# Optimization experiments

Hardware: AMD Instinct MI355X
Metric: run time of the kernel (lower is better)

Reference implementation:

```python
import jax, jax.numpy as jnp
import numpy as np

N, E, IN, H, G = 100000, 1600000, 64, 108, 128
N_LAYERS = 2  # hidden_dims=[108,108] -> 1 layer from hidden_dims[1:] + 1 final layer


def setup_inputs() -> dict:
    key = jax.random.key(0)
    ks = jax.random.split(key, 13)
    s = lambda fan_in: 1.0 / np.sqrt(fan_in)
    inp = {
        "nodes_feat": jax.random.normal(ks[0], (N, IN), jnp.float32),
        "edges_feat": jax.random.normal(ks[1], (E, 1), jnp.float32),
        "nodes_num_norm_sqrt": jax.random.uniform(ks[2], (N,), jnp.float32),
        "edges_num_norm_sqrt": jax.random.uniform(ks[3], (E,), jnp.float32),
        "W_emb": jax.random.uniform(ks[4], (IN, H), jnp.float32, -s(IN), s(IN)),
        "b_emb": jax.random.uniform(ks[5], (H,), jnp.float32, -s(IN), s(IN)),
        "pool_W": jax.random.uniform(ks[6], (N_LAYERS, H, H), jnp.float32, -s(H), s(H)),
        "pool_b": jax.random.uniform(ks[7], (N_LAYERS, H), jnp.float32, -s(H), s(H)),
        "app_W": jax.random.uniform(ks[8], (N_LAYERS, 2 * H, H), jnp.float32, -s(2 * H), s(2 * H)),
        "app_b": jax.random.uniform(ks[9], (N_LAYERS, H), jnp.float32, -s(2 * H), s(2 * H)),
        "src": jax.random.randint(ks[10], (E,), 0, N, jnp.int64 if jax.config.jax_enable_x64 else jnp.int32),
        "dst": jax.random.randint(ks[11], (E,), 0, N, jnp.int64 if jax.config.jax_enable_x64 else jnp.int32),
        "graph_ids": jnp.sort(jax.random.randint(ks[12], (N,), 0, G, jnp.int64 if jax.config.jax_enable_x64 else jnp.int32)),
        "n_graphs": G,
    }
    return inp


def reference(nodes_feat, edges_feat, nodes_num_norm_sqrt, edges_num_norm_sqrt,
              W_emb, b_emb, pool_W, pool_b, app_W, app_b,
              src, dst, graph_ids, n_graphs):
    n = nodes_feat.shape[0]
    # embedding_h
    h = nodes_feat @ W_emb + b_emb  # [N, H]
    # in-degree for mean aggregation (dropout = 0.0 so omitted)
    deg = jax.ops.segment_sum(jnp.ones((src.shape[0],), h.dtype), dst, num_segments=n)
    deg = jnp.maximum(deg, 1.0)[:, None]  # [N, 1]
    for i in range(pool_W.shape[0]):
        h_in = h
        # meanpool aggregator: per-message linear+ReLU == per-node transform then gather
        z = jax.nn.relu(h @ pool_W[i] + pool_b[i])  # [N, H]
        c = jax.ops.segment_sum(z[src], dst, num_segments=n) / deg  # mean over neighbors
        # NodeApply: linear(concat(h, c)) -> L2 normalize -> activation
        b = jnp.concatenate([h, c], axis=1) @ app_W[i] + app_b[i]
        b = b / jnp.maximum(jnp.linalg.norm(b, axis=1, keepdims=True), 1e-12)
        h = h_in + jax.nn.relu(b)  # residual (dims match: 108 == 108)
    # dgl.mean_nodes readout per graph
    cnt = jax.ops.segment_sum(jnp.ones((n,), h.dtype), graph_ids, num_segments=n_graphs)
    hg = jax.ops.segment_sum(h, graph_ids, num_segments=n_graphs) / jnp.maximum(cnt, 1.0)[:, None]
    return hg  # [n_graphs, H]
```

## Files before the change

kernel.cpp:

```cpp
#include <hip/hip_runtime.h>

#define HDIM 108
constexpr int G_GRAPHS = 128;
constexpr int MAXNB = 1024;
constexpr int CAP = 2560;

typedef _Float16 half8 __attribute__((ext_vector_type(8)));
typedef _Float16 half4v __attribute__((ext_vector_type(4)));
typedef float floatx4 __attribute__((ext_vector_type(4)));
typedef float floatx2 __attribute__((ext_vector_type(2)));

__device__ inline unsigned char f32_to_fp8(float t) {
#if __has_builtin(__builtin_amdgcn_cvt_pk_fp8_f32)
  return (unsigned char)(__builtin_amdgcn_cvt_pk_fp8_f32(t, t, 0, false) & 0xFF);
#else
  t = fminf(t, 448.f);
  if (t < 0.015625f) return (unsigned char)__float2int_rn(t * 512.f);
  unsigned u = __float_as_uint(t);
  unsigned lsb = (u >> 20) & 1;
  u += 0x7FFFFu + lsb;
  int e = (int)((u >> 23) & 0xFF) - 127;
  if (e > 8) return 0x7E;
  return (unsigned char)(((e + 7) << 3) | ((u >> 20) & 7));
#endif
}

template <bool HI>
__device__ inline floatx2 fp8x2_to_f32(unsigned v) {
#if __has_builtin(__builtin_amdgcn_cvt_pk_f32_fp8)
  return __builtin_amdgcn_cvt_pk_f32_fp8((int)v, HI);
#else
  unsigned b0 = HI ? ((v >> 16) & 0xFF) : (v & 0xFF);
  unsigned b1 = HI ? ((v >> 24) & 0xFF) : ((v >> 8) & 0xFF);
  floatx2 r;
  {
    unsigned s = b0 >> 7, e = (b0 >> 3) & 0xF, m = b0 & 7;
    float f = (e == 0) ? (float)m * 0.001953125f
                       : __uint_as_float(((e + 120u) << 23) | (m << 20));
    r[0] = s ? -f : f;
  }
  {
    unsigned s = b1 >> 7, e = (b1 >> 3) & 0xF, m = b1 & 7;
    float f = (e == 0) ? (float)m * 0.001953125f
                       : __uint_as_float(((e + 120u) << 23) | (m << 20));
    r[1] = s ? -f : f;
  }
  return r;
#endif
}

__global__ __launch_bounds__(1024) void k_fused0(const int* __restrict__ src, const int* __restrict__ dst,
                                                 int* __restrict__ gcur, int* __restrict__ ebuf,
                                                 const float* __restrict__ pool_W,
                                                 const float* __restrict__ app_W,
                                                 _Float16* __restrict__ wtp,
                                                 _Float16* __restrict__ wta,
                                                 const float* __restrict__ feat,
                                                 const float* __restrict__ W_emb,
                                                 const float* __restrict__ b_emb,
                                                 _Float16* __restrict__ h16,
                                                 int E, int nb, int nsc, int N) {
  __shared__ __align__(16) char smraw[29440];
  const int tid = threadIdx.x;

  if ((int)blockIdx.x < nsc) {
    int* hist = (int*)smraw;
    const int e0 = blockIdx.x * 16384;

    int gi = blockIdx.x * 1024 + tid;
    if (gi < 78848) {
      const float* srcw;
      _Float16* dstw;
      int Kpad, split, rel;
      if (gi < 14336)      { rel = gi;          srcw = pool_W;         dstw = wtp;         Kpad = 128; split = 0; }
      else if (gi < 28672) { rel = gi - 14336;  srcw = pool_W + 11664; dstw = wtp + 14336; Kpad = 128; split = 0; }
      else if (gi < 53760) { rel = gi - 28672;  srcw = app_W;          dstw = wta;         Kpad = 224; split = 1; }
      else                 { rel = gi - 53760;  srcw = app_W + 23328;  dstw = wta + 25088; Kpad = 224; split = 1; }
      int n = rel / Kpad, k = rel - n * Kpad;
      int ks;
      if (split) ks = (k < 108) ? k : (k >= 112 && k < 220) ? (k - 4) : -1;
      else       ks = (k < 108) ? k : -1;
      float v = (n < 108 && ks >= 0) ? srcw[ks * 108 + n] : 0.f;
      dstw[rel] = (_Float16)v;
    }

    for (int b = tid; b < nb; b += 1024) hist[b] = 0;
    __syncthreads();
#pragma unroll
    for (int it = 0; it < 16; it++) {
      int e = e0 + it * 1024 + tid;
      if (e < E) atomicAdd(&hist[dst[e] >> 7], 1);
    }
    __syncthreads();
    for (int b = tid; b < nb; b += 1024) {
      int h = hist[b];
      hist[b] = h ? atomicAdd(&gcur[b * 16], h) : 0;
    }
    __syncthreads();
#pragma unroll
    for (int it = 0; it < 16; it++) {
      int e = e0 + it * 1024 + tid;
      if (e < E) {
        int d = dst[e];
        int b = d >> 7;
        int rank = atomicAdd(&hist[b], 1);
        if (rank < CAP) ebuf[(size_t)b * CAP + rank] = src[e] | ((d & 127) << 20);
      }
    }
  } else {
    _Float16* As = (_Float16*)smraw;
    _Float16* Ws = (_Float16*)(smraw + 20480);
    const int sub = tid >> 8;
    const int stid = tid & 255;
    const int swave = stid >> 6;
    const int slane = stid & 63;
    const int lo = slane & 15;
    const int quad = slane >> 4;
    const int n0 = (((int)blockIdx.x - nsc) * 4 + sub) * 64;

    floatx4 acc[7];
#pragma unroll
    for (int ct = 0; ct < 7; ct++) {
      floatx4 zz = {0.f, 0.f, 0.f, 0.f};
      acc[ct] = zz;
    }

#pragma unroll 1
    for (int kc = 0; kc < 2; kc++) {
      {
        int r = stid >> 2, sg = stid & 3;
        int gn = n0 + r;
        int k = kc * 32 + sg * 8;
        half8 v = {0, 0, 0, 0, 0, 0, 0, 0};
        if (gn < N) {
          float4 f0 = *(const float4*)(feat + (size_t)gn * 64 + k);
          float4 f1 = *(const float4*)(feat + (size_t)gn * 64 + k + 4);
          v[0] = (_Float16)f0.x; v[1] = (_Float16)f0.y; v[2] = (_Float16)f0.z; v[3] = (_Float16)f0.w;
          v[4] = (_Float16)f1.x; v[5] = (_Float16)f1.y; v[6] = (_Float16)f1.z; v[7] = (_Float16)f1.w;
        }
        *(half8*)&As[sub * 2560 + r * 40 + sg * 8] = v;
      }
      if (tid < 448) {
        int nrow = tid >> 2, sg = tid & 3;
        int kb = kc * 32 + sg * 8;
        half8 v = {0, 0, 0, 0, 0, 0, 0, 0};
        if (nrow < 108) {
#pragma unroll
          for (int j = 0; j < 8; j++) v[j] = (_Float16)W_emb[(kb + j) * 108 + nrow];
        }
        *(half8*)&Ws[nrow * 40 + sg * 8] = v;
      }
      __syncthreads();

      half8 a = *(const half8*)&As[sub * 2560 + (swave * 16 + lo) * 40 + quad * 8];
#pragma unroll
      for (int ct = 0; ct < 7; ct++) {
        half8 b = *(const half8*)&Ws[(ct * 16 + lo) * 40 + quad * 8];
        acc[ct] = __builtin_amdgcn_mfma_f32_16x16x32_f16(a, b, acc[ct], 0, 0, 0);
      }
      __syncthreads();
    }

    float bias_v[7];
#pragma unroll
    for (int ct = 0; ct < 7; ct++) {
      int col = ct * 16 + lo;
      bias_v[ct] = (col < 108) ? b_emb[col] : 0.f;
    }
#pragma unroll
    for (int reg = 0; reg < 4; reg++) {
      int gr = n0 + swave * 16 + quad * 4 + reg;
      if (gr < N) {
        _Float16* op = h16 + (size_t)gr * 112 + lo;
#pragma unroll
        for (int ct = 0; ct < 7; ct++) {
          float t = acc[ct][reg] + bias_v[ct];
          op[ct * 16] = (_Float16)t;
        }
      }
    }
  }
}

__global__ __launch_bounds__(1024) void k_bagg(const unsigned char* __restrict__ z, const int* __restrict__ ebuf,
                                               const int* __restrict__ gcur, _Float16* __restrict__ c16,
                                               int N, int nb) {
  __shared__ int cnts[128];
  __shared__ int scanb[128];
  __shared__ int off[129];
  __shared__ int ecur[128];
  __shared__ int esrc[CAP];
  const int tid = threadIdx.x;
  const int b = blockIdx.x;
  const int v0 = b << 7;
  int cntb = gcur[b * 16];
  if (cntb > CAP) cntb = CAP;
  const int* eb = ebuf + (size_t)b * CAP;

  if (tid < 128) cnts[tid] = 0;
  __syncthreads();
  for (int i = tid; i < cntb; i += 1024) atomicAdd(&cnts[eb[i] >> 20], 1);
  __syncthreads();
  if (tid < 128) scanb[tid] = cnts[tid];
  __syncthreads();
#pragma unroll
  for (int st = 1; st < 128; st <<= 1) {
    int v = 0;
    if (tid < 128 && tid >= st) v = scanb[tid - st];
    __syncthreads();
    if (tid < 128) scanb[tid] += v;
    __syncthreads();
  }
  if (tid == 0) off[0] = 0;
  if (tid < 128) {
    off[tid + 1] = scanb[tid];
    ecur[tid] = scanb[tid] - cnts[tid];
  }
  __syncthreads();
  for (int i = tid; i < cntb; i += 1024) {
    int e = eb[i];
    int p = atomicAdd(&ecur[e >> 20], 1);
    esrc[p] = e & 0xFFFFF;
  }
  __syncthreads();

  const int lane = tid & 31;
  const int grp = tid >> 5;
  if (lane >= 28) return;
  const unsigned char* __restrict__ zl = z + lane * 4;
#pragma unroll 1
  for (int r = grp; r < 128; r += 32) {
    int v = v0 + r;
    if (v >= N) continue;
    int s = off[r], e2 = off[r + 1];
    float a0 = 0.f, a1 = 0.f, a2 = 0.f, a3 = 0.f;
    int j = s;
    for (; j + 4 <= e2; j += 4) {
      unsigned q0 = *(const unsigned*)(zl + (size_t)esrc[j] * 128);
      unsigned q1 = *(const unsigned*)(zl + (size_t)esrc[j + 1] * 128);
      unsigned q2 = *(const unsigned*)(zl + (size_t)esrc[j + 2] * 128);
      unsigned q3 = *(const unsigned*)(zl + (size_t)esrc[j + 3] * 128);
      floatx2 l0 = fp8x2_to_f32<false>(q0), h0 = fp8x2_to_f32<true>(q0);
      floatx2 l1 = fp8x2_to_f32<false>(q1), h1 = fp8x2_to_f32<true>(q1);
      floatx2 l2 = fp8x2_to_f32<false>(q2), h2 = fp8x2_to_f32<true>(q2);
      floatx2 l3 = fp8x2_to_f32<false>(q3), h3 = fp8x2_to_f32<true>(q3);
      a0 += (l0[0] + l1[0]) + (l2[0] + l3[0]);
      a1 += (l0[1] + l1[1]) + (l2[1] + l3[1]);
      a2 += (h0[0] + h1[0]) + (h2[0] + h3[0]);
      a3 += (h0[1] + h1[1]) + (h2[1] + h3[1]);
    }
    for (; j < e2; j++) {
      unsigned q0 = *(const unsigned*)(zl + (size_t)esrc[j] * 128);
      floatx2 l0 = fp8x2_to_f32<false>(q0), h0 = fp8x2_to_f32<true>(q0);
      a0 += l0[0]; a1 += l0[1]; a2 += h0[0]; a3 += h0[1];
    }
    int d = e2 - s;
    float inv = 1.f / (float)(d > 0 ? d : 1);
    half4v r4;
    r4[0] = (_Float16)(a0 * inv); r4[1] = (_Float16)(a1 * inv);
    r4[2] = (_Float16)(a2 * inv); r4[3] = (_Float16)(a3 * inv);
    *(half4v*)(c16 + (size_t)v * 112 + lane * 4) = r4;
  }
}

template <int KCH, int MODE>
__global__ __launch_bounds__(256) void k_mmf(const void* Asrc, const _Float16* __restrict__ c16,
                                             const _Float16* __restrict__ Wt, const float* __restrict__ bias,
                                             void* outp, int N) {
  constexpr int KW = KCH * 32;
  __shared__ _Float16 As[64 * 40];
  __shared__ _Float16 Ws[112 * 40];

  const int tid = threadIdx.x;
  const int wave = tid >> 6;
  const int lane = tid & 63;
  const int lo = lane & 15;
  const int quad = lane >> 4;
  const int n0 = blockIdx.x * 64;
  const _Float16* h16 = (const _Float16*)Asrc;

  floatx4 acc[7];
#pragma unroll
  for (int ct = 0; ct < 7; ct++) {
    floatx4 zz = {0.f, 0.f, 0.f, 0.f};
    acc[ct] = zz;
  }

#pragma unroll 1
  for (int kc = 0; kc < KCH; kc++) {
    {
      int r = tid >> 2, sg = tid & 3;
      int gn = n0 + r;
      int k = kc * 32 + sg * 8;
      half8 v = {0, 0, 0, 0, 0, 0, 0, 0};
      if (gn < N) {
        if (MODE == 2) {
          const _Float16* sp = (k < 112) ? (h16 + (size_t)gn * 112 + k)
                                         : (c16 + (size_t)gn * 112 + (k - 112));
          v = *(const half8*)sp;
        } else {
          if (k < 112) v = *(const half8*)(h16 + (size_t)gn * 112 + k);
        }
      }
      *(half8*)&As[r * 40 + sg * 8] = v;
    }
#pragma unroll
    for (int it = 0; it < 2; it++) {
      int idx = tid + it * 256;
      if (idx < 448) {
        int nrow = idx >> 2, sg = idx & 3;
        half8 v = *(const half8*)(Wt + (size_t)nrow * KW + kc * 32 + sg * 8);
        *(half8*)&Ws[nrow * 40 + sg * 8] = v;
      }
    }
    __syncthreads();

    half8 a = *(const half8*)&As[(wave * 16 + lo) * 40 + quad * 8];
#pragma unroll
    for (int ct = 0; ct < 7; ct++) {
      half8 b = *(const half8*)&Ws[(ct * 16 + lo) * 40 + quad * 8];
      acc[ct] = __builtin_amdgcn_mfma_f32_16x16x32_f16(a, b, acc[ct], 0, 0, 0);
    }
    __syncthreads();
  }

  float bias_v[7];
#pragma unroll
  for (int ct = 0; ct < 7; ct++) {
    int col = ct * 16 + lo;
    bias_v[ct] = (col < 108) ? bias[col] : 0.f;
  }

  if (MODE == 2) {
    _Float16* out16 = (_Float16*)outp;
#pragma unroll
    for (int reg = 0; reg < 4; reg++) {
      int gr = n0 + wave * 16 + quad * 4 + reg;
      float bv[7];
      float ssq = 0.f;
#pragma unroll
      for (int ct = 0; ct < 7; ct++) {
        float t = acc[ct][reg] + bias_v[ct];
        bv[ct] = t;
        ssq += t * t;
      }
#pragma unroll
      for (int s = 1; s < 16; s <<= 1) ssq += __shfl_xor(ssq, s, 16);
      float scale = 1.f / fmaxf(sqrtf(ssq), 1e-12f);
      if (gr < N) {
        _Float16* hp = out16 + (size_t)gr * 112 + lo;
#pragma unroll
        for (int ct = 0; ct < 7; ct++) {
          float hv = (float)hp[ct * 16];
          hp[ct * 16] = (_Float16)(hv + fmaxf(bv[ct] * scale, 0.f));
        }
      }
    }
  } else {
    unsigned char* outb = (unsigned char*)outp;
#pragma unroll
    for (int reg = 0; reg < 4; reg++) {
      int gr = n0 + wave * 16 + quad * 4 + reg;
      if (gr < N) {
        unsigned char* op = outb + (size_t)gr * 128 + lo;
#pragma unroll
        for (int ct = 0; ct < 7; ct++) {
          float t = fmaxf(acc[ct][reg] + bias_v[ct], 0.f);
          op[ct * 16] = f32_to_fp8(t);
        }
      }
    }
  }
}

__global__ __launch_bounds__(256) void k_readout(const _Float16* __restrict__ h, const int* __restrict__ gid,
                                                 float* __restrict__ hg, int N) {
  const int CH = 16;
  const int lane = threadIdx.x & 31;
  const int grp = threadIdx.x >> 5;
  int start = (blockIdx.x * 8 + grp) * CH;
  if (start >= N || lane >= 27) return;
  int end = min(start + CH, N);
  float a0 = 0.f, a1 = 0.f, a2 = 0.f, a3 = 0.f;
  int cur = gid[start];
  for (int i = start; i < end; i++) {
    int g = gid[i];
    if (g != cur) {
      float* base = &hg[(size_t)cur * HDIM + lane * 4];
      atomicAdd(base + 0, a0); atomicAdd(base + 1, a1);
      atomicAdd(base + 2, a2); atomicAdd(base + 3, a3);
      a0 = a1 = a2 = a3 = 0.f;
      cur = g;
    }
    half4v v = *(const half4v*)(h + (size_t)i * 112 + lane * 4);
    a0 += (float)v[0]; a1 += (float)v[1]; a2 += (float)v[2]; a3 += (float)v[3];
  }
  float* base = &hg[(size_t)cur * HDIM + lane * 4];
  atomicAdd(base + 0, a0); atomicAdd(base + 1, a1);
  atomicAdd(base + 2, a2); atomicAdd(base + 3, a3);
}

__global__ __launch_bounds__(256) void k_div(const float* __restrict__ hg, const int* __restrict__ gid,
                                             float* __restrict__ out, int total, int N) {
  int i = blockIdx.x * 256 + threadIdx.x;
  if (i < total) {
    int g = i / HDIM;
    int lo = 0, hi = N;
    while (lo < hi) { int m = (lo + hi) >> 1; if (gid[m] < g) lo = m + 1; else hi = m; }
    int lb = lo;
    lo = 0; hi = N;
    while (lo < hi) { int m = (lo + hi) >> 1; if (gid[m] <= g) lo = m + 1; else hi = m; }
    int c = lo - lb;
    out[i] = hg[i] / (float)(c > 0 ? c : 1);
  }
}

extern "C" void kernel_launch(void* const* d_in, const int* in_sizes, int n_in,
                              void* d_out, int out_size, void* d_ws, size_t ws_size,
                              hipStream_t stream) {
  (void)n_in; (void)ws_size; (void)out_size;
  const float* nodes_feat = (const float*)d_in[0];
  const float* W_emb = (const float*)d_in[4];
  const float* b_emb = (const float*)d_in[5];
  const float* pool_W = (const float*)d_in[6];
  const float* pool_b = (const float*)d_in[7];
  const float* app_W = (const float*)d_in[8];
  const float* app_b = (const float*)d_in[9];
  const int* src = (const int*)d_in[10];
  const int* dst = (const int*)d_in[11];
  const int* gid = (const int*)d_in[12];
  const int N = in_sizes[2];
  const int E = in_sizes[10];
  float* out = (float*)d_out;

  const int nb = (N + 127) >> 7;
  const int nbMM = (N + 63) / 64;
  const int nsc = (E + 16383) / 16384;
  const int ngb = (nbMM + 3) / 4;

  char* ws = (char*)d_ws;
  size_t off = 0;
  auto alloc = [&](size_t bytes) -> size_t {
    size_t o = off;
    off += (bytes + 1023) & ~size_t(1023);
    return o;
  };
  size_t o_gcur = alloc((size_t)MAXNB * 16 * 4);
  size_t o_hg   = alloc((size_t)G_GRAPHS * HDIM * 4);
  size_t zero_bytes = off;
  size_t o_ebuf = alloc((size_t)MAXNB * CAP * 4);
  size_t o_h  = alloc((size_t)N * 112 * 2);
  size_t o_z  = alloc((size_t)N * 128);
  size_t o_c  = alloc((size_t)N * 112 * 2);
  size_t o_wp = alloc((size_t)2 * 112 * 128 * 2);
  size_t o_wa = alloc((size_t)2 * 112 * 224 * 2);

  int*           gcur = (int*)(ws + o_gcur);
  float*         hg   = (float*)(ws + o_hg);
  int*           ebuf = (int*)(ws + o_ebuf);
  _Float16*      h16  = (_Float16*)(ws + o_h);
  unsigned char* z8   = (unsigned char*)(ws + o_z);
  _Float16*      c16  = (_Float16*)(ws + o_c);
  _Float16*      wtp  = (_Float16*)(ws + o_wp);
  _Float16*      wta  = (_Float16*)(ws + o_wa);

  (void)hipMemsetAsync(d_ws, 0, zero_bytes, stream);

  k_fused0<<<nsc + ngb, 1024, 0, stream>>>(src, dst, gcur, ebuf,
                                           pool_W, app_W, wtp, wta,
                                           nodes_feat, W_emb, b_emb, h16,
                                           E, nb, nsc, N);

  for (int i = 0; i < 2; i++) {
    k_mmf<4, 1><<<nbMM, 256, 0, stream>>>(h16, nullptr, wtp + i * 14336,
                                          pool_b + i * HDIM, z8, N);
    k_bagg<<<nb, 1024, 0, stream>>>(z8, ebuf, gcur, c16, N, nb);
    k_mmf<7, 2><<<nbMM, 256, 0, stream>>>(h16, c16, wta + i * 25088,
                                          app_b + i * HDIM, h16, N);
  }

  k_readout<<<(N + 8 * 16 - 1) / (8 * 16), 256, 0, stream>>>(h16, gid, hg, N);
  k_div<<<(G_GRAPHS * HDIM + 255) / 256, 256, 0, stream>>>(hg, gid, out, G_GRAPHS * HDIM, N);
}
```

Measured before the change: 328.6 us.

## Double-buffer LDS tiles in k_mmf and halve k_bagg block size

The matmul kernel now uses two LDS buffers. The next K-chunk of A and W is loaded into registers while the MFMAs run on the current chunk, which removes one barrier per iteration and hides global-load latency. The aggregation kernel drops from 1024 to 512 threads per block, with each wave group handling twice as many rows, which may improve occupancy or scheduling. Double buffering doubles LDS use and raises register pressure, and the smaller bagg blocks have less parallelism per block.

New measurement: 312.1 us. -5.0%, faster.

```diff
diff --git a/kernel.cpp b/kernel.cpp
--- a/kernel.cpp
+++ b/kernel.cpp
@@ -182,9 +182,9 @@
   }
 }
 
-__global__ __launch_bounds__(1024) void k_bagg(const unsigned char* __restrict__ z, const int* __restrict__ ebuf,
-                                               const int* __restrict__ gcur, _Float16* __restrict__ c16,
-                                               int N, int nb) {
+__global__ __launch_bounds__(512) void k_bagg(const unsigned char* __restrict__ z, const int* __restrict__ ebuf,
+                                              const int* __restrict__ gcur, _Float16* __restrict__ c16,
+                                              int N, int nb) {
   __shared__ int cnts[128];
   __shared__ int scanb[128];
   __shared__ int off[129];
@@ -199,7 +199,7 @@
 
   if (tid < 128) cnts[tid] = 0;
   __syncthreads();
-  for (int i = tid; i < cntb; i += 1024) atomicAdd(&cnts[eb[i] >> 20], 1);
+  for (int i = tid; i < cntb; i += 512) atomicAdd(&cnts[eb[i] >> 20], 1);
   __syncthreads();
   if (tid < 128) scanb[tid] = cnts[tid];
   __syncthreads();
@@ -217,7 +217,7 @@
     ecur[tid] = scanb[tid] - cnts[tid];
   }
   __syncthreads();
-  for (int i = tid; i < cntb; i += 1024) {
+  for (int i = tid; i < cntb; i += 512) {
     int e = eb[i];
     int p = atomicAdd(&ecur[e >> 20], 1);
     esrc[p] = e & 0xFFFFF;
@@ -229,7 +229,7 @@
   if (lane >= 28) return;
   const unsigned char* __restrict__ zl = z + lane * 4;
 #pragma unroll 1
-  for (int r = grp; r < 128; r += 32) {
+  for (int r = grp; r < 128; r += 16) {
     int v = v0 + r;
     if (v >= N) continue;
     int s = off[r], e2 = off[r + 1];
@@ -268,8 +268,8 @@
                                              const _Float16* __restrict__ Wt, const float* __restrict__ bias,
                                              void* outp, int N) {
   constexpr int KW = KCH * 32;
-  __shared__ _Float16 As[64 * 40];
-  __shared__ _Float16 Ws[112 * 40];
+  __shared__ _Float16 As[2][64 * 40];
+  __shared__ _Float16 Ws[2][112 * 40];
 
   const int tid = threadIdx.x;
   const int wave = tid >> 6;
@@ -279,6 +279,37 @@
   const int n0 = blockIdx.x * 64;
   const _Float16* h16 = (const _Float16*)Asrc;
 
+  const int ar = tid >> 2, asg = tid & 3;
+  const int gnA = n0 + ar;
+  const int wrow0 = tid >> 2, wsg0 = tid & 3;
+  const int widx1 = tid + 256;
+  const int wrow1 = widx1 >> 2, wsg1 = widx1 & 3;
+
+  auto loadA = [&](int kc) -> half8 {
+    int k = kc * 32 + asg * 8;
+    half8 v = {0, 0, 0, 0, 0, 0, 0, 0};
+    if (gnA < N) {
+      if (MODE == 2) {
+        const _Float16* sp = (k < 112) ? (h16 + (size_t)gnA * 112 + k)
+                                       : (c16 + (size_t)gnA * 112 + (k - 112));
+        v = *(const half8*)sp;
+      } else {
+        if (k < 112) v = *(const half8*)(h16 + (size_t)gnA * 112 + k);
+      }
+    }
+    return v;
+  };
+
+  half8 aR = loadA(0);
+  half8 wR0 = *(const half8*)(Wt + (size_t)wrow0 * KW + wsg0 * 8);
+  half8 wR1 = {0, 0, 0, 0, 0, 0, 0, 0};
+  if (tid < 192) wR1 = *(const half8*)(Wt + (size_t)wrow1 * KW + wsg1 * 8);
+
+  *(half8*)&As[0][ar * 40 + asg * 8] = aR;
+  *(half8*)&Ws[0][wrow0 * 40 + wsg0 * 8] = wR0;
+  if (tid < 192) *(half8*)&Ws[0][wrow1 * 40 + wsg1 * 8] = wR1;
+  __syncthreads();
+
   floatx4 acc[7];
 #pragma unroll
   for (int ct = 0; ct < 7; ct++) {
@@ -288,40 +319,26 @@
 
 #pragma unroll 1
   for (int kc = 0; kc < KCH; kc++) {
-    {
-      int r = tid >> 2, sg = tid & 3;
-      int gn = n0 + r;
-      int k = kc * 32 + sg * 8;
-      half8 v = {0, 0, 0, 0, 0, 0, 0, 0};
-      if (gn < N) {
-        if (MODE == 2) {
-          const _Float16* sp = (k < 112) ? (h16 + (size_t)gn * 112 + k)
-                                         : (c16 + (size_t)gn * 112 + (k - 112));
-          v = *(const half8*)sp;
-        } else {
-          if (k < 112) v = *(const half8*)(h16 + (size_t)gn * 112 + k);
-        }
-      }
-      *(half8*)&As[r * 40 + sg * 8] = v;
-    }
-#pragma unroll
-    for (int it = 0; it < 2; it++) {
-      int idx = tid + it * 256;
-      if (idx < 448) {
-        int nrow = idx >> 2, sg = idx & 3;
-        half8 v = *(const half8*)(Wt + (size_t)nrow * KW + kc * 32 + sg * 8);
-        *(half8*)&Ws[nrow * 40 + sg * 8] = v;
-      }
-    }
-    __syncthreads();
-
-    half8 a = *(const half8*)&As[(wave * 16 + lo) * 40 + quad * 8];
+    const int cur = kc & 1, nxt = cur ^ 1;
+    if (kc + 1 < KCH) {
+      aR = loadA(kc + 1);
+      wR0 = *(const half8*)(Wt + (size_t)wrow0 * KW + (kc + 1) * 32 + wsg0 * 8);
+      if (tid < 192) wR1 = *(const half8*)(Wt + (size_t)wrow1 * KW + (kc + 1) * 32 + wsg1 * 8);
+    }
+
+    half8 a = *(const half8*)&As[cur][(wave * 16 + lo) * 40 + quad * 8];
 #pragma unroll
     for (int ct = 0; ct < 7; ct++) {
-      half8 b = *(const half8*)&Ws[(ct * 16 + lo) * 40 + quad * 8];
+      half8 b = *(const half8*)&Ws[cur][(ct * 16 + lo) * 40 + quad * 8];
       acc[ct] = __builtin_amdgcn_mfma_f32_16x16x32_f16(a, b, acc[ct], 0, 0, 0);
     }
-    __syncthreads();
+
+    if (kc + 1 < KCH) {
+      *(half8*)&As[nxt][ar * 40 + asg * 8] = aR;
+      *(half8*)&Ws[nxt][wrow0 * 40 + wsg0 * 8] = wR0;
+      if (tid < 192) *(half8*)&Ws[nxt][wrow1 * 40 + wsg1 * 8] = wR1;
+      __syncthreads();
+    }
   }
 
   float bias_v[7];
@@ -474,7 +491,7 @@
   for (int i = 0; i < 2; i++) {
     k_mmf<4, 1><<<nbMM, 256, 0, stream>>>(h16, nullptr, wtp + i * 14336,
                                           pool_b + i * HDIM, z8, N);
-    k_bagg<<<nb, 1024, 0, stream>>>(z8, ebuf, gcur, c16, N, nb);
+    k_bagg<<<nb, 512, 0, stream>>>(z8, ebuf, gcur, c16, N, nb);
     k_mmf<7, 2><<<nbMM, 256, 0, stream>>>(h16, c16, wta + i * 25088,
                                           app_b + i * HDIM, h16, N);
   }
```
